# Performance work log

Hardware: AMD Instinct MI355X
Metric: run time of the kernel (lower is better)

## Reference

```python
import jax, jax.numpy as jnp
import numpy as np

B, N, D = 4, 1024, 1024
H = 16
RS, RC = 32, 32
MLP = int(D * 4.0)
EPS = 1e-6


def _ln(x):
    # LayerNorm with no scale/bias (flax defaults: eps=1e-6)
    m = jnp.mean(x, axis=-1, keepdims=True)
    v = jnp.mean(jnp.square(x - m), axis=-1, keepdims=True)
    return (x - m) * jax.lax.rsqrt(v + EPS)


def _rms(x, scale):
    rms = jnp.sqrt(jnp.mean(jnp.square(x), axis=-1, keepdims=True) + EPS)
    return scale * x / rms


def _modulate(x, shift, scale):
    return x * (1 + scale[:, None]) + shift[:, None]


def setup_inputs() -> dict:
    key = jax.random.key(0)
    ks = jax.random.split(key, 20)
    s = 0.02
    return {
        'x': jax.random.normal(ks[0], (B, N, D), jnp.float32),
        'c': jax.random.normal(ks[1], (B, D), jnp.float32),
        'cls_token': jax.random.normal(ks[2], (B, D), jnp.float32),
        'Wc': jax.random.normal(ks[3], (D, 6 * D), jnp.float32) * s,
        'bc': jax.random.normal(ks[4], (6 * D,), jnp.float32) * s,
        'Wqkv': jax.random.normal(ks[5], (D, 3 * D), jnp.float32) * s,
        'bqkv': jnp.zeros((3 * D,), jnp.float32),
        'Wo': jax.random.normal(ks[6], (D, D), jnp.float32) * s,
        'bo': jnp.zeros((D,), jnp.float32),
        'A_s': jax.random.normal(ks[7], (D, RS), jnp.float32) * s,
        'B_s': jax.random.normal(ks[8], (RS, D), jnp.float32) * s,
        'rms_s_scale': jnp.ones((D,), jnp.float32),
        'C_r': jax.random.normal(ks[9], (D, RC), jnp.float32) * s,
        'D_r': jax.random.normal(ks[10], (RC, D), jnp.float32) * s,
        'rms_c_scale': jnp.ones((D,), jnp.float32),
        'W1': jax.random.normal(ks[11], (D, MLP), jnp.float32) * s,
        'b1': jnp.zeros((MLP,), jnp.float32),
        'W2': jax.random.normal(ks[12], (MLP, D), jnp.float32) * s,
        'b2': jnp.zeros((D,), jnp.float32),
    }


def reference(x, c, cls_token, Wc, bc, Wqkv, bqkv, Wo, bo, A_s, B_s,
              rms_s_scale, C_r, D_r, rms_c_scale, W1, b1, W2, b2):
    hd = D // H
    # AdaLN conditioning
    c_proj = jax.nn.silu(c) @ Wc + bc                    # (B, 6D)
    shift_a, scale_a, gate_a, shift_m, scale_m, gate_m = jnp.split(c_proj, 6, axis=-1)

    # Self-attention branch
    x_norm = _modulate(_ln(x), shift_a, scale_a)         # (B, N, D)
    qkv = x_norm @ Wqkv + bqkv                           # (B, N, 3D)
    q, k, v = jnp.split(qkv, 3, axis=-1)
    q = q.reshape(B, N, H, hd).transpose(0, 2, 1, 3)     # (B, H, N, hd)
    k = k.reshape(B, N, H, hd).transpose(0, 2, 1, 3)
    v = v.reshape(B, N, H, hd).transpose(0, 2, 1, 3)
    attn_w = jax.nn.softmax(jnp.einsum('bhqd,bhkd->bhqk', q, k) * hd ** (-0.5), axis=-1)
    attn_out = jnp.einsum('bhqk,bhkd->bhqd', attn_w, v)
    attn_out = attn_out.transpose(0, 2, 1, 3).reshape(B, N, D)
    attn_out = attn_out @ Wo + bo
    Y = x + gate_a[:, None] * attn_out

    # Self-gram low-rank branch (residual)
    gram_s = (x @ A_s) @ B_s                             # (B, N, D)
    X_prime = _rms(gram_s, rms_s_scale) + Y

    # Cross-gram branch via CLS token (no residual)
    u_c = cls_token[:, :, None] * C_r[None]              # (B, D, RC)
    v_c = jnp.einsum('bnd,bdr->bnr', X_prime, u_c)       # (B, N, RC)
    gram_c = v_c @ D_r                                   # (B, N, D)
    Z = _rms(gram_c, rms_c_scale)

    # MLP branch
    z_norm = _modulate(_ln(Z), shift_m, scale_m)
    h = jax.nn.gelu(z_norm @ W1 + b1) @ W2 + b2
    return Z + gate_m[:, None] * h
```

## Files before the change

kernel.cpp:

```cpp
#include <hip/hip_runtime.h>
#include <stdint.h>

typedef float  f32x4  __attribute__((ext_vector_type(4)));
typedef int    i32x4  __attribute__((ext_vector_type(4)));
typedef __bf16 bf16x4 __attribute__((ext_vector_type(4)));

#define D_    1024
#define SIXD  6144
#define QSCALE 0.18033688011112042f

#define BAR() asm volatile("s_barrier" ::: "memory")

__device__ __forceinline__ void mfma16(const i32x4 &a, const i32x4 &b, f32x4 &c) {
  asm("v_mfma_f32_16x16x32_bf16 %0, %1, %2, %0" : "+v"(c) : "v"(a), "v"(b));
}

__device__ __forceinline__ void gload_lds16(const void* g, void* l) {
  __builtin_amdgcn_global_load_lds(
      (const __attribute__((address_space(1))) uint32_t*)g,
      (__attribute__((address_space(3))) uint32_t*)l, 16, 0, 0);
}

__global__ __launch_bounds__(256)
void cond_gemm(const float* __restrict__ c, const float* __restrict__ Wc,
               const float* __restrict__ bc, float* __restrict__ cproj)
{
  __shared__ float sc[4096];
  __shared__ float tp[8][4][32];
  int tid = threadIdx.x;
  for (int i = tid; i < 4096; i += 256) {
    float v = c[i];
    sc[i] = v / (1.f + __expf(-v));
  }
  __syncthreads();
  int colo = tid & 31, kseg = tid >> 5;
  int col = blockIdx.x * 32 + colo;
  float a0 = 0.f, a1 = 0.f, a2 = 0.f, a3 = 0.f;
  for (int k = kseg * 128; k < kseg * 128 + 128; k++) {
    float w = Wc[(size_t)k * SIXD + col];
    a0 += sc[k] * w; a1 += sc[1024 + k] * w;
    a2 += sc[2048 + k] * w; a3 += sc[3072 + k] * w;
  }
  tp[kseg][0][colo] = a0; tp[kseg][1][colo] = a1;
  tp[kseg][2][colo] = a2; tp[kseg][3][colo] = a3;
  __syncthreads();
  if (kseg == 0) {
#pragma unroll
    for (int b = 0; b < 4; b++) {
      float s = bc[col];
#pragma unroll
      for (int g = 0; g < 8; g++) s += tp[g][b][colo];
      cproj[b * SIXD + col] = s;
    }
  }
}

__global__ __launch_bounds__(256)
void transpose_all(const float* __restrict__ Wqkv, const float* __restrict__ Wo,
                   const float* __restrict__ W1, const float* __restrict__ W2,
                   __bf16* __restrict__ Wqkvt, __bf16* __restrict__ Wot,
                   __bf16* __restrict__ W1t, __bf16* __restrict__ W2t)
{
  __shared__ __bf16 t[64][65];
  int bid = blockIdx.x;
  const float* W; __bf16* Wt; int Kdim, Ndim, lb;
  if (bid < 768)       { W = Wqkv; Wt = Wqkvt; Kdim = 1024; Ndim = 3072; lb = bid; }
  else if (bid < 1024) { W = Wo;   Wt = Wot;   Kdim = 1024; Ndim = 1024; lb = bid - 768; }
  else if (bid < 2048) { W = W1;   Wt = W1t;   Kdim = 1024; Ndim = 4096; lb = bid - 1024; }
  else                 { W = W2;   Wt = W2t;   Kdim = 4096; Ndim = 1024; lb = bid - 2048; }
  int ntn = Ndim >> 6;
  int kt = lb / ntn, nt = lb % ntn;
  int tid = threadIdx.x;
  const float* src = W + (size_t)(kt * 64) * Ndim + nt * 64;
#pragma unroll
  for (int i = 0; i < 4; i++) {
    int k = i * 16 + (tid >> 4);
    int c4 = tid & 15;
    float4 v = ((const float4*)(src + (size_t)k * Ndim))[c4];
    t[k][c4 * 4 + 0] = (__bf16)v.x; t[k][c4 * 4 + 1] = (__bf16)v.y;
    t[k][c4 * 4 + 2] = (__bf16)v.z; t[k][c4 * 4 + 3] = (__bf16)v.w;
  }
  __syncthreads();
  __bf16* dst = Wt + (size_t)(nt * 64) * Kdim + kt * 64;
  int n = tid >> 2, ks = (tid & 3) * 16;
  bf16x4 o0, o1, o2, o3;
#pragma unroll
  for (int j = 0; j < 4; j++) {
    o0[j] = t[ks + j][n];      o1[j] = t[ks + 4 + j][n];
    o2[j] = t[ks + 8 + j][n];  o3[j] = t[ks + 12 + j][n];
  }
  __bf16* dp = dst + (size_t)n * Kdim + ks;
  *(bf16x4*)(dp) = o0; *(bf16x4*)(dp + 4) = o1;
  *(bf16x4*)(dp + 8) = o2; *(bf16x4*)(dp + 12) = o3;
}

__global__ __launch_bounds__(256)
void transpose_v(const __bf16* __restrict__ qkv, __bf16* __restrict__ Vt)
{
  __shared__ __bf16 t[32][33];
  int bid = blockIdx.x;
  int dt = bid & 1, nt = (bid >> 1) & 31, bh = bid >> 6;
  int b = bh >> 4, h = bh & 15;
  int x = threadIdx.x & 31, yq = threadIdx.x >> 5;
  const __bf16* src = qkv + ((size_t)(b * 1024 + nt * 32)) * 3072 + 2048 + h * 64 + dt * 32;
#pragma unroll
  for (int i = 0; i < 4; i++) {
    int row = yq * 4 + i;
    t[row][x] = src[(size_t)row * 3072 + x];
  }
  __syncthreads();
  __bf16* dst = Vt + ((size_t)(bh * 64 + dt * 32)) * 1024 + nt * 32;
#pragma unroll
  for (int i = 0; i < 4; i++) {
    int drow = yq * 4 + i;
    dst[(size_t)drow * 1024 + x] = t[x][drow];
  }
}

__global__ __launch_bounds__(256)
void ln_mod(const float* __restrict__ X, const float* __restrict__ cproj,
            int shift_off, int scale_off, __bf16* __restrict__ Out)
{
  int row = blockIdx.x;
  int b = row >> 10;
  int tid = threadIdx.x;
  const float4* xr = (const float4*)(X + (size_t)row * D_);
  float4 v = xr[tid];
  float s  = v.x + v.y + v.z + v.w;
  float s2 = v.x * v.x + v.y * v.y + v.z * v.z + v.w * v.w;
#pragma unroll
  for (int off = 1; off < 64; off <<= 1) {
    s  += __shfl_xor(s,  off, 64);
    s2 += __shfl_xor(s2, off, 64);
  }
  __shared__ float red[8];
  int wave = tid >> 6, lane = tid & 63;
  if (lane == 0) { red[wave] = s; red[4 + wave] = s2; }
  __syncthreads();
  s  = red[0] + red[1] + red[2] + red[3];
  s2 = red[4] + red[5] + red[6] + red[7];
  float mean = s * (1.f / D_);
  float var  = s2 * (1.f / D_) - mean * mean;
  float rstd = rsqrtf(var + 1e-6f);
  const float4* sh = (const float4*)(cproj + b * SIXD + shift_off);
  const float4* sc = (const float4*)(cproj + b * SIXD + scale_off);
  float4 shv = sh[tid], scv = sc[tid];
  bf16x4 o;
  o[0] = (__bf16)((v.x - mean) * rstd * (1.f + scv.x) + shv.x);
  o[1] = (__bf16)((v.y - mean) * rstd * (1.f + scv.y) + shv.y);
  o[2] = (__bf16)((v.z - mean) * rstd * (1.f + scv.z) + shv.z);
  o[3] = (__bf16)((v.w - mean) * rstd * (1.f + scv.w) + shv.w);
  *(bf16x4*)(Out + (size_t)row * D_ + tid * 4) = o;
}

template<int EPI, int NBUF>
__global__ __launch_bounds__(256)
void gemm_bt(const __bf16* __restrict__ A, const __bf16* __restrict__ Bt,
             const float* __restrict__ bias, const float* __restrict__ cproj,
             int gate_off, const float* __restrict__ resid,
             void* __restrict__ Cout, void* __restrict__ Cout2,
             void* __restrict__ Cout3, void* __restrict__ Cout4,
             int M, int N, int K, int SK)
{
  __shared__ __align__(16) __bf16 As[NBUF * 128 * 32];
  __shared__ __align__(16) __bf16 Bs[NBUF * 128 * 32];
  const int PD = NBUF - 1;
  int tilesN = N >> 7, tilesM = M >> 7;
  int npersk = tilesM * tilesN;
  int sk = blockIdx.x / npersk;
  int rest = blockIdx.x % npersk;
  int cpx = npersk >> 3;
  rest = (rest & 7) * cpx + (rest >> 3);
  int bm = rest / tilesN, bn = rest % tilesN;
  int Klen = K / SK, Kstart = sk * Klen;

  int tid = threadIdx.x;
  int lane = tid & 63, wave = tid >> 6;
  int lr = lane & 15, lg = lane >> 4;
  int wm = (wave >> 1) << 6, wn = (wave & 1) << 6;

  f32x4 acc[4][4] = {};

  int sr = tid >> 2, skb = tid & 3;
  int scol = ((skb ^ ((sr >> 1) & 3)) * 8);
  const __bf16* pa = A + (size_t)((bm << 7) + sr) * K + Kstart + scol;
  const __bf16* pb = Bt + (size_t)((bn << 7) + sr) * K + Kstart + scol;
  const size_t rstep = (size_t)64 * K;
  __bf16* la = As + tid * 8;
  __bf16* lb = Bs + tid * 8;

  auto STAGE = [&](int buf, int k0) {
    int bo = buf * 4096;
    gload_lds16(pa + k0, la + bo);
    gload_lds16(pa + rstep + k0, la + bo + 2048);
    gload_lds16(pb + k0, lb + bo);
    gload_lds16(pb + rstep + k0, lb + bo + 2048);
  };

  int nt = Klen >> 5;
#pragma unroll
  for (int p = 0; p < PD; p++) STAGE(p, p * 32);

  for (int t = 0; t < nt; t++) {
    if (t + PD < nt) STAGE((t + PD) % NBUF, (t + PD) * 32);
    int ahead = nt - 1 - t; if (ahead > PD) ahead = PD;
    if (ahead >= 3)      asm volatile("s_waitcnt vmcnt(12)" ::: "memory");
    else if (ahead == 2) asm volatile("s_waitcnt vmcnt(8)" ::: "memory");
    else if (ahead == 1) asm volatile("s_waitcnt vmcnt(4)" ::: "memory");
    else                 asm volatile("s_waitcnt vmcnt(0)" ::: "memory");
    BAR();
    const __bf16* Ac = As + (t % NBUF) * 4096;
    const __bf16* Bc = Bs + (t % NBUF) * 4096;
    i32x4 af[4], bfv[4];
#pragma unroll
    for (int m = 0; m < 4; m++) {
      int row = wm + m * 16 + lr;
      af[m] = *(const i32x4*)(Ac + row * 32 + ((lg ^ ((row >> 1) & 3)) * 8));
    }
#pragma unroll
    for (int n = 0; n < 4; n++) {
      int row = wn + n * 16 + lr;
      bfv[n] = *(const i32x4*)(Bc + row * 32 + ((lg ^ ((row >> 1) & 3)) * 8));
    }
    asm volatile("s_waitcnt lgkmcnt(0)" ::: "memory");
    __builtin_amdgcn_sched_barrier(0);
    BAR();
    __builtin_amdgcn_s_setprio(1);
#pragma unroll
    for (int m = 0; m < 4; m++)
#pragma unroll
      for (int n = 0; n < 4; n++)
        mfma16(af[m], bfv[n], acc[m][n]);
    __builtin_amdgcn_s_setprio(0);
  }
  asm volatile("s_waitcnt vmcnt(0)" ::: "memory");
  asm volatile("s_nop 7\n\ts_nop 7" ::);

  __bf16* Pp = nullptr;
  if (EPI == 3) {
    if (sk == 0)      Pp = (__bf16*)Cout;
    else if (sk == 1) Pp = (__bf16*)Cout2;
    else if (sk == 2) Pp = (__bf16*)Cout3;
    else              Pp = (__bf16*)Cout4;
  }

  int row0 = (bm << 7) + wm;
  int col0 = (bn << 7) + wn;
#pragma unroll
  for (int m = 0; m < 4; m++) {
#pragma unroll
    for (int n = 0; n < 4; n++) {
      int cc = col0 + n * 16 + lr;
      float bv = (EPI == 3) ? 0.f : bias[cc];
#pragma unroll
      for (int r = 0; r < 4; r++) {
        int row = row0 + m * 16 + (lg << 2) + r;
        float v = acc[m][n][r] + bv;
        size_t idx = (size_t)row * N + cc;
        if (EPI == 0) {
          ((__bf16*)Cout)[idx] = (__bf16)v;
        } else if (EPI == 1) {
          int b = row >> 10;
          float g = cproj[b * SIXD + gate_off + cc];
          ((float*)Cout)[idx] = resid[idx] + g * v;
        } else if (EPI == 2) {
          float u = 0.7978845608028654f * (v + 0.044715f * v * v * v);
          u = fminf(fmaxf(u, -15.f), 15.f);
          float e = __expf(2.f * u);
          float th = (e - 1.f) / (e + 1.f);
          ((__bf16*)Cout)[idx] = (__bf16)(0.5f * v * (1.f + th));
        } else if (EPI == 4) {
          float scq = (cc < 1024) ? QSCALE : 1.f;
          ((__bf16*)Cout)[idx] = (__bf16)(v * scq);
        } else {
          Pp[idx] = (__bf16)v;
        }
      }
    }
  }
}

template<int EPI>
__global__ __launch_bounds__(512, 2)
void gemm256(const __bf16* __restrict__ A, const __bf16* __restrict__ Bt,
             const float* __restrict__ bias,
             void* __restrict__ Cout, void* __restrict__ Cout2,
             void* __restrict__ Cout3, void* __restrict__ Cout4,
             int M, int N, int K, int SK)
{
  __shared__ __align__(16) __bf16 As[2 * 16384];
  __shared__ __align__(16) __bf16 Bs[2 * 16384];
  int tilesN = N >> 8, tilesM = M >> 8;
  int npersk = tilesM * tilesN;
  int sk = blockIdx.x / npersk;
  int rest = blockIdx.x % npersk;
  int cpx = npersk >> 3;
  rest = (rest & 7) * cpx + (rest >> 3);
  int bm = rest / tilesN, bn = rest % tilesN;
  int Klen = K / SK, Kstart = sk * Klen;
  int nt = Klen >> 6;

  int tid = threadIdx.x;
  int lane = tid & 63, wave = tid >> 6;
  int lr = lane & 15, lg = lane >> 4;
  int wr = wave >> 2, wc = wave & 3;

  f32x4 acc[8][4] = {};

  int srow = tid >> 3;
  int schunk = (tid & 7) ^ (srow & 7);
  const __bf16* pa = A  + (size_t)((bm << 8) + srow) * K + Kstart + schunk * 8;
  const __bf16* pb = Bt + (size_t)((bn << 8) + srow) * K + Kstart + schunk * 8;
  __bf16* la = As + tid * 8;
  __bf16* lb = Bs + tid * 8;

  auto SA = [&](int t, int h, int j) {
    gload_lds16(pa + (size_t)(h * 128 + j * 64) * K + t * 64,
                la + (t & 1) * 16384 + h * 8192 + j * 4096);
  };
  auto SB = [&](int t, int h, int j) {
    gload_lds16(pb + (size_t)(h * 128 + j * 64) * K + t * 64,
                lb + (t & 1) * 16384 + h * 8192 + j * 4096);
  };

  SA(0,0,0); SA(0,0,1); SA(0,1,0); SA(0,1,1);
  SB(0,0,0); SB(0,0,1); SB(0,1,0); SB(0,1,1);
  SB(1,0,0); SB(1,0,1); SB(1,1,0); SB(1,1,1);
  asm volatile("s_waitcnt vmcnt(4)" ::: "memory");
  BAR();

  int cc0 = ((lg ^ (lr & 7)) << 4);
  int cc1 = cc0 ^ 64;
  const char* aA = (const char*)As + (wr * 128 + lr) * 128;
  const char* aB = (const char*)Bs + (wc * 64 + lr) * 128;

  i32x4 af[4][2], b0[2][2], b1[2][2];
  for (int t = 0; t < nt; t++) {
    const char* Ab = aA + (t & 1) * 32768;
    const char* Bb = aB + (t & 1) * 32768;

#pragma unroll
    for (int m = 0; m < 4; m++) {
      af[m][0] = *(const i32x4*)(Ab + m * 2048 + cc0);
      af[m][1] = *(const i32x4*)(Ab + m * 2048 + cc1);
    }
#pragma unroll
    for (int n = 0; n < 2; n++) {
      b0[n][0] = *(const i32x4*)(Bb + n * 2048 + cc0);
      b0[n][1] = *(const i32x4*)(Bb + n * 2048 + cc1);
    }
    if (t + 1 < nt) { SA(t + 1, 0, 0); SA(t + 1, 0, 1); }
    BAR();
    asm volatile("s_waitcnt lgkmcnt(0)" ::: "memory");
    __builtin_amdgcn_sched_barrier(0);
    __builtin_amdgcn_s_setprio(1);
#pragma unroll
    for (int m = 0; m < 4; m++)
#pragma unroll
      for (int n = 0; n < 2; n++) {
        mfma16(af[m][0], b0[n][0], acc[m][n]);
        mfma16(af[m][1], b0[n][1], acc[m][n]);
      }
    __builtin_amdgcn_s_setprio(0);
    BAR();

#pragma unroll
    for (int n = 0; n < 2; n++) {
      b1[n][0] = *(const i32x4*)(Bb + 4096 + n * 2048 + cc0);
      b1[n][1] = *(const i32x4*)(Bb + 4096 + n * 2048 + cc1);
    }
    if (t + 1 < nt) { SA(t + 1, 1, 0); SA(t + 1, 1, 1); }
    BAR();
    asm volatile("s_waitcnt lgkmcnt(0)" ::: "memory");
    __builtin_amdgcn_sched_barrier(0);
    __builtin_amdgcn_s_setprio(1);
#pragma unroll
    for (int m = 0; m < 4; m++)
#pragma unroll
      for (int n = 0; n < 2; n++) {
        mfma16(af[m][0], b1[n][0], acc[m][2 + n]);
        mfma16(af[m][1], b1[n][1], acc[m][2 + n]);
      }
    __builtin_amdgcn_s_setprio(0);
    BAR();

#pragma unroll
    for (int m = 0; m < 4; m++) {
      af[m][0] = *(const i32x4*)(Ab + 8192 + m * 2048 + cc0);
      af[m][1] = *(const i32x4*)(Ab + 8192 + m * 2048 + cc1);
    }
    if (t + 2 < nt) { SB(t + 2, 0, 0); SB(t + 2, 0, 1); }
    BAR();
    asm volatile("s_waitcnt lgkmcnt(0)" ::: "memory");
    __builtin_amdgcn_sched_barrier(0);
    __builtin_amdgcn_s_setprio(1);
#pragma unroll
    for (int m = 0; m < 4; m++)
#pragma unroll
      for (int n = 0; n < 2; n++) {
        mfma16(af[m][0], b1[n][0], acc[4 + m][2 + n]);
        mfma16(af[m][1], b1[n][1], acc[4 + m][2 + n]);
      }
    __builtin_amdgcn_s_setprio(0);
    BAR();

    if (t + 2 < nt) {
      SB(t + 2, 1, 0); SB(t + 2, 1, 1);
      asm volatile("s_waitcnt vmcnt(4)" ::: "memory");
    } else {
      asm volatile("s_waitcnt vmcnt(0)" ::: "memory");
    }
    BAR();
    __builtin_amdgcn_s_setprio(1);
#pragma unroll
    for (int m = 0; m < 4; m++)
#pragma unroll
      for (int n = 0; n < 2; n++) {
        mfma16(af[m][0], b0[n][0], acc[4 + m][n]);
        mfma16(af[m][1], b0[n][1], acc[4 + m][n]);
      }
    __builtin_amdgcn_s_setprio(0);
    BAR();
  }
  asm volatile("s_nop 7\n\ts_nop 7" ::);

  __bf16* Pp = nullptr;
  if (EPI == 3) {
    if (sk == 0)      Pp = (__bf16*)Cout;
    else if (sk == 1) Pp = (__bf16*)Cout2;
    else if (sk == 2) Pp = (__bf16*)Cout3;
    else              Pp = (__bf16*)Cout4;
  }

  int row0 = (bm << 8) + wr * 128;
  int col0 = (bn << 8) + wc * 64;
#pragma unroll
  for (int m = 0; m < 8; m++) {
#pragma unroll
    for (int n = 0; n < 4; n++) {
      int cc = col0 + n * 16 + lr;
      float bv = (EPI == 3) ? 0.f : bias[cc];
#pragma unroll
      for (int r = 0; r < 4; r++) {
        int row = row0 + m * 16 + (lg << 2) + r;
        float v = acc[m][n][r] + bv;
        size_t idx = (size_t)row * N + cc;
        if (EPI == 2) {
          float u = 0.7978845608028654f * (v + 0.044715f * v * v * v);
          u = fminf(fmaxf(u, -15.f), 15.f);
          float e = __expf(2.f * u);
          float th = (e - 1.f) / (e + 1.f);
          ((__bf16*)Cout)[idx] = (__bf16)(0.5f * v * (1.f + th));
        } else if (EPI == 4) {
          float scq = (cc < 1024) ? QSCALE : 1.f;
          ((__bf16*)Cout)[idx] = (__bf16)(v * scq);
        } else {
          Pp[idx] = (__bf16)v;
        }
      }
    }
  }
}

__global__ __launch_bounds__(256)
void reduce_w2(const __bf16* __restrict__ P0, const __bf16* __restrict__ P1,
               const __bf16* __restrict__ P2, const __bf16* __restrict__ P3,
               const float* __restrict__ bias, const float* __restrict__ cproj,
               float* __restrict__ Out)
{
  int row = blockIdx.x;
  int b = row >> 10;
  int tid = threadIdx.x;
  size_t base = (size_t)row * D_ + tid * 4;
  bf16x4 a0 = *(const bf16x4*)(P0 + base);
  bf16x4 a1 = *(const bf16x4*)(P1 + base);
  bf16x4 a2 = *(const bf16x4*)(P2 + base);
  bf16x4 a3 = *(const bf16x4*)(P3 + base);
  f32x4 s;
#pragma unroll
  for (int i = 0; i < 4; i++)
    s[i] = ((float)a0[i] + (float)a1[i]) + ((float)a2[i] + (float)a3[i]);
  f32x4 bz = *(const f32x4*)(bias + tid * 4);
  f32x4 g  = *(const f32x4*)(cproj + b * SIXD + 5120 + tid * 4);
  f32x4 z  = *(const f32x4*)(Out + base);
  *(f32x4*)(Out + base) = z + g * (s + bz);
}

__global__ __launch_bounds__(512, 4)
void attn_flash(const __bf16* __restrict__ qkv, const __bf16* __restrict__ Vt,
                __bf16* __restrict__ O)
{
  __shared__ __align__(16) __bf16 Kl[2][64 * 64];
  __shared__ __align__(16) __bf16 Vl[2][64 * 64];
  __shared__ __align__(16) __bf16 Pl[8][16 * 64];

  int bid = ((blockIdx.x & 7) << 6) | (blockIdx.x >> 3);
  int qt = bid & 7, h = (bid >> 3) & 15, b = bid >> 7;
  int tid = threadIdx.x, wave = tid >> 6, lane = tid & 63;
  int lr = lane & 15, lg = lane >> 4;

  size_t tok0 = (size_t)b * 1024;
  int qrow = qt * 128 + wave * 16 + lr;
  const __bf16* qptr = qkv + (tok0 + qrow) * 3072 + h * 64;
  i32x4 qf0 = *(const i32x4*)(qptr + lg * 8);
  i32x4 qf1 = *(const i32x4*)(qptr + 32 + lg * 8);

  float l_acc[4] = {0.f, 0.f, 0.f, 0.f};
  f32x4 oacc[4] = {};

  const __bf16* kbase = qkv + tok0 * 3072 + 1024 + h * 64;
  const __bf16* vbase = Vt + ((size_t)(b * 16 + h) * 64) * 1024;

  int skey = tid >> 3, sdb = tid & 7;
  const __bf16* ksrc = kbase + (size_t)skey * 3072 + ((sdb ^ (skey & 7)) * 8);
  const __bf16* vsrc = vbase + (size_t)skey * 1024 + ((sdb ^ (skey & 7)) * 8);
  __bf16* klp = &Kl[0][0] + tid * 8;
  __bf16* vlp = &Vl[0][0] + tid * 8;
  __bf16* pl = &Pl[wave][0];

  auto STAGE = [&](int buf, int kk) {
    gload_lds16(ksrc + (size_t)kk * 3072, klp + buf * 4096);
    gload_lds16(vsrc + kk, vlp + buf * 4096);
  };

  STAGE(0, 0);
  int cur = 0;
  for (int k0 = 0; k0 < 1024; k0 += 64) {
    int kn = (k0 + 64 < 1024) ? (k0 + 64) : k0;
    STAGE(cur ^ 1, kn);
    asm volatile("s_waitcnt vmcnt(2)" ::: "memory");
    BAR();
    const __bf16* K_ = &Kl[cur][0];
    const __bf16* V_ = &Vl[cur][0];

    f32x4 s[4];
    __builtin_amdgcn_s_setprio(1);
#pragma unroll
    for (int n = 0; n < 4; n++) {
      int key = n * 16 + lr;
      int kx = key & 7;
      i32x4 kf0 = *(const i32x4*)(K_ + key * 64 + ((lg ^ kx) * 8));
      i32x4 kf1 = *(const i32x4*)(K_ + key * 64 + (((4 + lg) ^ kx) * 8));
      f32x4 sa = {0.f, 0.f, 0.f, 0.f};
      mfma16(qf0, kf0, sa);
      mfma16(qf1, kf1, sa);
      s[n] = sa;
    }
    __builtin_amdgcn_s_setprio(0);

#pragma unroll
    for (int n = 0; n < 4; n++)
#pragma unroll
      for (int r = 0; r < 4; r++)
        s[n][r] = exp2f(s[n][r]);
#pragma unroll
    for (int r = 0; r < 4; r++)
      l_acc[r] += (s[0][r] + s[1][r]) + (s[2][r] + s[3][r]);

#pragma unroll
    for (int n = 0; n < 4; n++)
#pragma unroll
      for (int r = 0; r < 4; r++) {
        int prow = lg * 4 + r;
        int key = n * 16 + lr;
        int idx = prow * 64 + (((key >> 3) ^ (prow & 7)) * 8) + (key & 7);
        pl[idx] = (__bf16)s[n][r];
      }
    asm volatile("s_waitcnt lgkmcnt(0)" ::: "memory");
    __builtin_amdgcn_sched_barrier(0);
    i32x4 pf0 = *(const i32x4*)(pl + lr * 64 + ((lg ^ (lr & 7)) * 8));
    i32x4 pf1 = *(const i32x4*)(pl + lr * 64 + (((4 + lg) ^ (lr & 7)) * 8));

    __builtin_amdgcn_s_setprio(1);
#pragma unroll
    for (int dt = 0; dt < 4; dt++) {
      int vrow = dt * 16 + lr, rx = vrow & 7;
      i32x4 vf0 = *(const i32x4*)(V_ + vrow * 64 + ((lg ^ rx) * 8));
      i32x4 vf1 = *(const i32x4*)(V_ + vrow * 64 + (((4 + lg) ^ rx) * 8));
      mfma16(pf0, vf0, oacc[dt]);
      mfma16(pf1, vf1, oacc[dt]);
    }
    __builtin_amdgcn_s_setprio(0);
    asm volatile("s_waitcnt lgkmcnt(0)" ::: "memory");
    __builtin_amdgcn_sched_barrier(0);
    BAR();
    cur ^= 1;
  }
  asm volatile("s_waitcnt vmcnt(0)" ::: "memory");
  asm volatile("s_nop 7\n\ts_nop 7" ::);

  float rinv[4];
#pragma unroll
  for (int r = 0; r < 4; r++) {
    float v = l_acc[r];
#pragma unroll
    for (int off = 1; off < 16; off <<= 1) v += __shfl_xor(v, off, 64);
    rinv[r] = 1.f / v;
  }

  int orow = qt * 128 + wave * 16 + (lg << 2);
#pragma unroll
  for (int dt = 0; dt < 4; dt++)
#pragma unroll
    for (int r = 0; r < 4; r++) {
      float v = oacc[dt][r] * rinv[r];
      O[(tok0 + orow + r) * 1024 + h * 64 + dt * 16 + lr] = (__bf16)v;
    }
}

__global__ __launch_bounds__(256)
void gram_fused(const float* __restrict__ X, const float* __restrict__ Y,
                const float* __restrict__ cls,
                const float* __restrict__ A_s, const float* __restrict__ B_s,
                const float* __restrict__ rms_s,
                const float* __restrict__ C_r, const float* __restrict__ D_r,
                const float* __restrict__ rms_c,
                const float* __restrict__ cproj,
                float* __restrict__ Z, __bf16* __restrict__ Znorm)
{
  __shared__ float xs[4][D_];
  __shared__ float tp[8][4][32];
  __shared__ float t1[4][32];
  __shared__ float red[4][4];
  __shared__ float red2[4][4][2];
  int row0 = blockIdx.x * 4;
  int b = row0 >> 10;
  int tid = threadIdx.x;
  int wv = tid >> 6;

  f32x4 cv = *(const f32x4*)(cls + (size_t)b * D_ + tid * 4);
  f32x4 yv[4];
#pragma unroll
  for (int rr = 0; rr < 4; rr++) {
    ((f32x4*)xs[rr])[tid] = *(const f32x4*)(X + (size_t)(row0 + rr) * D_ + tid * 4);
    yv[rr] = *(const f32x4*)(Y + (size_t)(row0 + rr) * D_ + tid * 4);
  }
  __syncthreads();

  {
    int r = tid & 31, seg = tid >> 5;
    float a0 = 0.f, a1 = 0.f, a2 = 0.f, a3 = 0.f;
    const float* ap = A_s + r;
    for (int d = seg * 128; d < seg * 128 + 128; d++) {
      float w = ap[d * 32];
      a0 += xs[0][d] * w; a1 += xs[1][d] * w;
      a2 += xs[2][d] * w; a3 += xs[3][d] * w;
    }
    tp[seg][0][r] = a0; tp[seg][1][r] = a1; tp[seg][2][r] = a2; tp[seg][3][r] = a3;
  }
  __syncthreads();
  if (tid < 128) {
    int rr = tid >> 5, r = tid & 31;
    float sv = 0.f;
#pragma unroll
    for (int g = 0; g < 8; g++) sv += tp[g][rr][r];
    t1[rr][r] = sv;
  }
  __syncthreads();

  f32x4 g[4] = {};
  for (int r = 0; r < 32; r++) {
    f32x4 bv = *(const f32x4*)(B_s + (size_t)r * D_ + tid * 4);
    g[0] += t1[0][r] * bv; g[1] += t1[1][r] * bv;
    g[2] += t1[2][r] * bv; g[3] += t1[3][r] * bv;
  }
  float ssl[4];
#pragma unroll
  for (int rr = 0; rr < 4; rr++)
    ssl[rr] = g[rr][0]*g[rr][0] + g[rr][1]*g[rr][1] + g[rr][2]*g[rr][2] + g[rr][3]*g[rr][3];
#pragma unroll
  for (int off = 1; off < 64; off <<= 1)
#pragma unroll
    for (int rr = 0; rr < 4; rr++) ssl[rr] += __shfl_xor(ssl[rr], off, 64);
  if ((tid & 63) == 0) {
#pragma unroll
    for (int rr = 0; rr < 4; rr++) red[wv][rr] = ssl[rr];
  }
  __syncthreads();
  {
    f32x4 scv = *(const f32x4*)(rms_s + tid * 4);
#pragma unroll
    for (int rr = 0; rr < 4; rr++) {
      float ss = red[0][rr] + red[1][rr] + red[2][rr] + red[3][rr];
      float rs = rsqrtf(ss * (1.f / D_) + 1e-6f);
      f32x4 xp = scv * g[rr] * rs + yv[rr];
      ((f32x4*)xs[rr])[tid] = xp * cv;
    }
  }
  __syncthreads();

  {
    int r = tid & 31, seg = tid >> 5;
    float a0 = 0.f, a1 = 0.f, a2 = 0.f, a3 = 0.f;
    const float* cp = C_r + r;
    for (int d = seg * 128; d < seg * 128 + 128; d++) {
      float w = cp[d * 32];
      a0 += xs[0][d] * w; a1 += xs[1][d] * w;
      a2 += xs[2][d] * w; a3 += xs[3][d] * w;
    }
    tp[seg][0][r] = a0; tp[seg][1][r] = a1; tp[seg][2][r] = a2; tp[seg][3][r] = a3;
  }
  __syncthreads();
  if (tid < 128) {
    int rr = tid >> 5, r = tid & 31;
    float sv = 0.f;
#pragma unroll
    for (int g2i = 0; g2i < 8; g2i++) sv += tp[g2i][rr][r];
    t1[rr][r] = sv;
  }
  __syncthreads();

  f32x4 g2[4] = {};
  for (int r = 0; r < 32; r++) {
    f32x4 bv = *(const f32x4*)(D_r + (size_t)r * D_ + tid * 4);
    g2[0] += t1[0][r] * bv; g2[1] += t1[1][r] * bv;
    g2[2] += t1[2][r] * bv; g2[3] += t1[3][r] * bv;
  }
#pragma unroll
  for (int rr = 0; rr < 4; rr++)
    ssl[rr] = g2[rr][0]*g2[rr][0] + g2[rr][1]*g2[rr][1] + g2[rr][2]*g2[rr][2] + g2[rr][3]*g2[rr][3];
#pragma unroll
  for (int off = 1; off < 64; off <<= 1)
#pragma unroll
    for (int rr = 0; rr < 4; rr++) ssl[rr] += __shfl_xor(ssl[rr], off, 64);
  if ((tid & 63) == 0) {
#pragma unroll
    for (int rr = 0; rr < 4; rr++) red[wv][rr] = ssl[rr];
  }
  __syncthreads();
  f32x4 z[4];
  {
    f32x4 scv = *(const f32x4*)(rms_c + tid * 4);
#pragma unroll
    for (int rr = 0; rr < 4; rr++) {
      float ss = red[0][rr] + red[1][rr] + red[2][rr] + red[3][rr];
      float rs = rsqrtf(ss * (1.f / D_) + 1e-6f);
      z[rr] = scv * g2[rr] * rs;
    }
  }

  float s1l[4], s2l[4];
#pragma unroll
  for (int rr = 0; rr < 4; rr++) {
    s1l[rr] = z[rr][0] + z[rr][1] + z[rr][2] + z[rr][3];
    s2l[rr] = z[rr][0]*z[rr][0] + z[rr][1]*z[rr][1] + z[rr][2]*z[rr][2] + z[rr][3]*z[rr][3];
  }
#pragma unroll
  for (int off = 1; off < 64; off <<= 1)
#pragma unroll
    for (int rr = 0; rr < 4; rr++) {
      s1l[rr] += __shfl_xor(s1l[rr], off, 64);
      s2l[rr] += __shfl_xor(s2l[rr], off, 64);
    }
  if ((tid & 63) == 0) {
#pragma unroll
    for (int rr = 0; rr < 4; rr++) { red2[wv][rr][0] = s1l[rr]; red2[wv][rr][1] = s2l[rr]; }
  }
  __syncthreads();
  f32x4 shv = *(const f32x4*)(cproj + b * SIXD + 3072 + tid * 4);
  f32x4 scm = *(const f32x4*)(cproj + b * SIXD + 4096 + tid * 4);
#pragma unroll
  for (int rr = 0; rr < 4; rr++) {
    float S  = red2[0][rr][0] + red2[1][rr][0] + red2[2][rr][0] + red2[3][rr][0];
    float S2 = red2[0][rr][1] + red2[1][rr][1] + red2[2][rr][1] + red2[3][rr][1];
    float mean = S * (1.f / D_);
    float var  = S2 * (1.f / D_) - mean * mean;
    float rstd = rsqrtf(var + 1e-6f);
    f32x4 zn = (z[rr] - mean) * rstd * (scm + 1.f) + shv;
    *(f32x4*)(Z + (size_t)(row0 + rr) * D_ + tid * 4) = z[rr];
    bf16x4 o;
#pragma unroll
    for (int i = 0; i < 4; i++) o[i] = (__bf16)zn[i];
    *(bf16x4*)(Znorm + (size_t)(row0 + rr) * D_ + tid * 4) = o;
  }
}

extern "C" void kernel_launch(void* const* d_in, const int* in_sizes, int n_in,
                              void* d_out, int out_size, void* d_ws, size_t ws_size,
                              hipStream_t stream)
{
  const float* x     = (const float*)d_in[0];
  const float* c     = (const float*)d_in[1];
  const float* cls   = (const float*)d_in[2];
  const float* Wc    = (const float*)d_in[3];
  const float* bc    = (const float*)d_in[4];
  const float* Wqkv  = (const float*)d_in[5];
  const float* bqkv  = (const float*)d_in[6];
  const float* Wo    = (const float*)d_in[7];
  const float* bo    = (const float*)d_in[8];
  const float* A_s   = (const float*)d_in[9];
  const float* B_s   = (const float*)d_in[10];
  const float* rms_s = (const float*)d_in[11];
  const float* C_r   = (const float*)d_in[12];
  const float* D_r   = (const float*)d_in[13];
  const float* rms_c = (const float*)d_in[14];
  const float* W1    = (const float*)d_in[15];
  const float* b1    = (const float*)d_in[16];
  const float* W2    = (const float*)d_in[17];
  const float* b2    = (const float*)d_in[18];
  float* out = (float*)d_out;

  float* ws = (float*)d_ws;
  __bf16* Wqkvt = (__bf16*)(ws + 0);
  __bf16* Wot   = (__bf16*)(ws + 1572864);
  __bf16* W1t   = (__bf16*)(ws + 2097152);
  __bf16* W2t   = (__bf16*)(ws + 4194304);
  float*  cproj = ws + 6291456;
  __bf16* xnorm = (__bf16*)(ws + 6316032);
  __bf16* qkv   = (__bf16*)(ws + 8413184);
  __bf16* Vt    = (__bf16*)(ws + 14704640);
  __bf16* h1    = (__bf16*)(ws + 8413184);
  __bf16* attno = (__bf16*)(ws + 16801792);
  float*  Ybuf  = ws + 18898944;
  __bf16* P0 = (__bf16*)(ws + 0);
  __bf16* P1 = (__bf16*)(ws + 2097152);
  __bf16* P2 = (__bf16*)(ws + 16801792);
  __bf16* P3 = (__bf16*)(ws + 18898944);

  cond_gemm<<<192, 256, 0, stream>>>(c, Wc, bc, cproj);
  transpose_all<<<3072, 256, 0, stream>>>(Wqkv, Wo, W1, W2, Wqkvt, Wot, W1t, W2t);
  ln_mod<<<4096, 256, 0, stream>>>(x, cproj, 0, 1024, xnorm);
  gemm256<4><<<192, 512, 0, stream>>>(xnorm, Wqkvt, bqkv,
                                      qkv, nullptr, nullptr, nullptr,
                                      4096, 3072, 1024, 1);
  transpose_v<<<4096, 256, 0, stream>>>(qkv, Vt);
  attn_flash<<<512, 512, 0, stream>>>(qkv, Vt, attno);
  gemm_bt<1, 4><<<256, 256, 0, stream>>>(attno, Wot, bo, cproj, 2048, x,
                                         Ybuf, nullptr, nullptr, nullptr,
                                         4096, 1024, 1024, 1);
  gram_fused<<<1024, 256, 0, stream>>>(x, Ybuf, cls, A_s, B_s, rms_s,
                                       C_r, D_r, rms_c, cproj, out, xnorm);
  gemm256<2><<<256, 512, 0, stream>>>(xnorm, W1t, b1,
                                      h1, nullptr, nullptr, nullptr,
                                      4096, 4096, 1024, 1);
  gemm256<3><<<256, 512, 0, stream>>>(h1, W2t, nullptr,
                                      P0, P1, P2, P3, 4096, 1024, 4096, 4);
  reduce_w2<<<4096, 256, 0, stream>>>(P0, P1, P2, P3, b2, cproj, out);
}
```

Before: 272.8 us.

## Restructure gemm256 main loop to prefetch LDS fragments and cut barriers

The gemm256 main loop is rewritten so A and B fragments for the next K-step are read from LDS at the end of the current step, and there are fewer barriers and no per-phase lgkmcnt waits. K length and K stride become template parameters, so the loop count and addresses are compile-time constants. Accumulators are moved to AGPRs through an MFMA variant with the 'a' constraint. The aim is to hide LDS latency and cut synchronisation stalls between MFMA phases. The cost is more register pressure and trickier vmcnt accounting for the double buffer.

```diff
diff --git a/kernel.cpp b/kernel.cpp
--- a/kernel.cpp
+++ b/kernel.cpp
@@ -13,6 +13,9 @@
 
 __device__ __forceinline__ void mfma16(const i32x4 &a, const i32x4 &b, f32x4 &c) {
   asm("v_mfma_f32_16x16x32_bf16 %0, %1, %2, %0" : "+v"(c) : "v"(a), "v"(b));
+}
+__device__ __forceinline__ void mfma16a(const i32x4 &a, const i32x4 &b, f32x4 &c) {
+  asm("v_mfma_f32_16x16x32_bf16 %0, %1, %2, %0" : "+a"(c) : "v"(a), "v"(b));
 }
 
 __device__ __forceinline__ void gload_lds16(const void* g, void* l) {
@@ -280,13 +283,13 @@
   }
 }
 
-template<int EPI>
+template<int EPI, int NT, int KD>
 __global__ __launch_bounds__(512, 2)
 void gemm256(const __bf16* __restrict__ A, const __bf16* __restrict__ Bt,
              const float* __restrict__ bias,
              void* __restrict__ Cout, void* __restrict__ Cout2,
              void* __restrict__ Cout3, void* __restrict__ Cout4,
-             int M, int N, int K, int SK)
+             int M, int N)
 {
   __shared__ __align__(16) __bf16 As[2 * 16384];
   __shared__ __align__(16) __bf16 Bs[2 * 16384];
@@ -297,8 +300,7 @@
   int cpx = npersk >> 3;
   rest = (rest & 7) * cpx + (rest >> 3);
   int bm = rest / tilesN, bn = rest % tilesN;
-  int Klen = K / SK, Kstart = sk * Klen;
-  int nt = Klen >> 6;
+  int Kstart = sk * (NT * 64);
 
   int tid = threadIdx.x;
   int lane = tid & 63, wave = tid >> 6;
@@ -309,23 +311,23 @@
 
   int srow = tid >> 3;
   int schunk = (tid & 7) ^ (srow & 7);
-  const __bf16* pa = A  + (size_t)((bm << 8) + srow) * K + Kstart + schunk * 8;
-  const __bf16* pb = Bt + (size_t)((bn << 8) + srow) * K + Kstart + schunk * 8;
+  const __bf16* pa = A  + (size_t)((bm << 8) + srow) * KD + Kstart + schunk * 8;
+  const __bf16* pb = Bt + (size_t)((bn << 8) + srow) * KD + Kstart + schunk * 8;
   __bf16* la = As + tid * 8;
   __bf16* lb = Bs + tid * 8;
 
-  auto SA = [&](int t, int h, int j) {
-    gload_lds16(pa + (size_t)(h * 128 + j * 64) * K + t * 64,
-                la + (t & 1) * 16384 + h * 8192 + j * 4096);
-  };
-  auto SB = [&](int t, int h, int j) {
-    gload_lds16(pb + (size_t)(h * 128 + j * 64) * K + t * 64,
-                lb + (t & 1) * 16384 + h * 8192 + j * 4096);
-  };
-
-  SA(0,0,0); SA(0,0,1); SA(0,1,0); SA(0,1,1);
-  SB(0,0,0); SB(0,0,1); SB(0,1,0); SB(0,1,1);
-  SB(1,0,0); SB(1,0,1); SB(1,1,0); SB(1,1,1);
+  gload_lds16(pa,                 la);
+  gload_lds16(pa + 64 * KD,       la + 4096);
+  gload_lds16(pa + 128 * KD,      la + 8192);
+  gload_lds16(pa + 192 * KD,      la + 12288);
+  gload_lds16(pb,                 lb);
+  gload_lds16(pb + 64 * KD,       lb + 4096);
+  gload_lds16(pb + 128 * KD,      lb + 8192);
+  gload_lds16(pb + 192 * KD,      lb + 12288);
+  gload_lds16(pb + 64,            lb + 16384);
+  gload_lds16(pb + 64 * KD + 64,  lb + 16384 + 4096);
+  gload_lds16(pb + 128 * KD + 64, lb + 16384 + 8192);
+  gload_lds16(pb + 192 * KD + 64, lb + 16384 + 12288);
   asm volatile("s_waitcnt vmcnt(4)" ::: "memory");
   BAR();
 
@@ -334,93 +336,112 @@
   const char* aA = (const char*)As + (wr * 128 + lr) * 128;
   const char* aB = (const char*)Bs + (wc * 64 + lr) * 128;
 
-  i32x4 af[4][2], b0[2][2], b1[2][2];
-  for (int t = 0; t < nt; t++) {
+  i32x4 alo[4][2], ahi[4][2], b0v[2][2], b1v[2][2];
+#pragma unroll
+  for (int m = 0; m < 4; m++) {
+    alo[m][0] = *(const i32x4*)(aA + m * 2048 + cc0);
+    alo[m][1] = *(const i32x4*)(aA + m * 2048 + cc1);
+  }
+#pragma unroll
+  for (int n = 0; n < 2; n++) {
+    b0v[n][0] = *(const i32x4*)(aB + n * 2048 + cc0);
+    b0v[n][1] = *(const i32x4*)(aB + n * 2048 + cc1);
+  }
+
+  for (int t = 0; t < NT; t++) {
     const char* Ab = aA + (t & 1) * 32768;
     const char* Bb = aB + (t & 1) * 32768;
-
-#pragma unroll
-    for (int m = 0; m < 4; m++) {
-      af[m][0] = *(const i32x4*)(Ab + m * 2048 + cc0);
-      af[m][1] = *(const i32x4*)(Ab + m * 2048 + cc1);
-    }
+    int nb = ((t + 1) & 1) * 16384;
+    int ob = (t & 1) * 16384;
+
 #pragma unroll
     for (int n = 0; n < 2; n++) {
-      b0[n][0] = *(const i32x4*)(Bb + n * 2048 + cc0);
-      b0[n][1] = *(const i32x4*)(Bb + n * 2048 + cc1);
-    }
-    if (t + 1 < nt) { SA(t + 1, 0, 0); SA(t + 1, 0, 1); }
-    BAR();
-    asm volatile("s_waitcnt lgkmcnt(0)" ::: "memory");
-    __builtin_amdgcn_sched_barrier(0);
+      b1v[n][0] = *(const i32x4*)(Bb + 4096 + n * 2048 + cc0);
+      b1v[n][1] = *(const i32x4*)(Bb + 4096 + n * 2048 + cc1);
+    }
+    if (t + 1 < NT) {
+      gload_lds16(pa + 64,            la + nb);
+      gload_lds16(pa + 128 * KD + 64, la + nb + 8192);
+    }
     __builtin_amdgcn_s_setprio(1);
 #pragma unroll
     for (int m = 0; m < 4; m++)
 #pragma unroll
       for (int n = 0; n < 2; n++) {
-        mfma16(af[m][0], b0[n][0], acc[m][n]);
-        mfma16(af[m][1], b0[n][1], acc[m][n]);
+        mfma16a(alo[m][0], b0v[n][0], acc[m][n]);
+        mfma16a(alo[m][1], b0v[n][1], acc[m][n]);
       }
     __builtin_amdgcn_s_setprio(0);
     BAR();
 
 #pragma unroll
-    for (int n = 0; n < 2; n++) {
-      b1[n][0] = *(const i32x4*)(Bb + 4096 + n * 2048 + cc0);
-      b1[n][1] = *(const i32x4*)(Bb + 4096 + n * 2048 + cc1);
-    }
-    if (t + 1 < nt) { SA(t + 1, 1, 0); SA(t + 1, 1, 1); }
-    BAR();
-    asm volatile("s_waitcnt lgkmcnt(0)" ::: "memory");
-    __builtin_amdgcn_sched_barrier(0);
+    for (int m = 0; m < 4; m++) {
+      ahi[m][0] = *(const i32x4*)(Ab + 8192 + m * 2048 + cc0);
+      ahi[m][1] = *(const i32x4*)(Ab + 8192 + m * 2048 + cc1);
+    }
+    if (t + 1 < NT) {
+      gload_lds16(pa + 64 * KD + 64,  la + nb + 4096);
+      gload_lds16(pa + 192 * KD + 64, la + nb + 12288);
+    }
     __builtin_amdgcn_s_setprio(1);
 #pragma unroll
     for (int m = 0; m < 4; m++)
 #pragma unroll
       for (int n = 0; n < 2; n++) {
-        mfma16(af[m][0], b1[n][0], acc[m][2 + n]);
-        mfma16(af[m][1], b1[n][1], acc[m][2 + n]);
+        mfma16a(alo[m][0], b1v[n][0], acc[m][2 + n]);
+        mfma16a(alo[m][1], b1v[n][1], acc[m][2 + n]);
       }
     __builtin_amdgcn_s_setprio(0);
     BAR();
 
-#pragma unroll
-    for (int m = 0; m < 4; m++) {
-      af[m][0] = *(const i32x4*)(Ab + 8192 + m * 2048 + cc0);
-      af[m][1] = *(const i32x4*)(Ab + 8192 + m * 2048 + cc1);
-    }
-    if (t + 2 < nt) { SB(t + 2, 0, 0); SB(t + 2, 0, 1); }
-    BAR();
-    asm volatile("s_waitcnt lgkmcnt(0)" ::: "memory");
-    __builtin_amdgcn_sched_barrier(0);
+    if (t + 2 < NT) {
+      gload_lds16(pb + 128,           lb + ob);
+      gload_lds16(pb + 64 * KD + 128, lb + ob + 4096);
+    }
     __builtin_amdgcn_s_setprio(1);
 #pragma unroll
     for (int m = 0; m < 4; m++)
 #pragma unroll
       for (int n = 0; n < 2; n++) {
-        mfma16(af[m][0], b1[n][0], acc[4 + m][2 + n]);
-        mfma16(af[m][1], b1[n][1], acc[4 + m][2 + n]);
+        mfma16a(ahi[m][0], b1v[n][0], acc[4 + m][2 + n]);
+        mfma16a(ahi[m][1], b1v[n][1], acc[4 + m][2 + n]);
       }
     __builtin_amdgcn_s_setprio(0);
+    if (t + 1 < NT) {
+      if (t + 2 < NT) asm volatile("s_waitcnt vmcnt(2)" ::: "memory");
+      else            asm volatile("s_waitcnt vmcnt(0)" ::: "memory");
+    }
     BAR();
 
-    if (t + 2 < nt) {
-      SB(t + 2, 1, 0); SB(t + 2, 1, 1);
-      asm volatile("s_waitcnt vmcnt(4)" ::: "memory");
-    } else {
-      asm volatile("s_waitcnt vmcnt(0)" ::: "memory");
-    }
-    BAR();
+    if (t + 2 < NT) {
+      gload_lds16(pb + 128 * KD + 128, lb + ob + 8192);
+      gload_lds16(pb + 192 * KD + 128, lb + ob + 12288);
+    }
     __builtin_amdgcn_s_setprio(1);
 #pragma unroll
     for (int m = 0; m < 4; m++)
 #pragma unroll
       for (int n = 0; n < 2; n++) {
-        mfma16(af[m][0], b0[n][0], acc[4 + m][n]);
-        mfma16(af[m][1], b0[n][1], acc[4 + m][n]);
+        mfma16a(ahi[m][0], b0v[n][0], acc[4 + m][n]);
+        mfma16a(ahi[m][1], b0v[n][1], acc[4 + m][n]);
       }
     __builtin_amdgcn_s_setprio(0);
+    if (t + 1 < NT) {
+      const char* An = aA + ((t + 1) & 1) * 32768;
+      const char* Bn = aB + ((t + 1) & 1) * 32768;
+#pragma unroll
+      for (int m = 0; m < 4; m++) {
+        alo[m][0] = *(const i32x4*)(An + m * 2048 + cc0);
+        alo[m][1] = *(const i32x4*)(An + m * 2048 + cc1);
+      }
+#pragma unroll
+      for (int n = 0; n < 2; n++) {
+        b0v[n][0] = *(const i32x4*)(Bn + n * 2048 + cc0);
+        b0v[n][1] = *(const i32x4*)(Bn + n * 2048 + cc1);
+      }
+    }
     BAR();
+    pa += 64; pb += 64;
   }
   asm volatile("s_nop 7\n\ts_nop 7" ::);
 
@@ -820,9 +841,9 @@
   cond_gemm<<<192, 256, 0, stream>>>(c, Wc, bc, cproj);
   transpose_all<<<3072, 256, 0, stream>>>(Wqkv, Wo, W1, W2, Wqkvt, Wot, W1t, W2t);
   ln_mod<<<4096, 256, 0, stream>>>(x, cproj, 0, 1024, xnorm);
-  gemm256<4><<<192, 512, 0, stream>>>(xnorm, Wqkvt, bqkv,
-                                      qkv, nullptr, nullptr, nullptr,
-                                      4096, 3072, 1024, 1);
+  gemm256<4, 16, 1024><<<192, 512, 0, stream>>>(xnorm, Wqkvt, bqkv,
+                                                qkv, nullptr, nullptr, nullptr,
+                                                4096, 3072);
   transpose_v<<<4096, 256, 0, stream>>>(qkv, Vt);
   attn_flash<<<512, 512, 0, stream>>>(qkv, Vt, attno);
   gemm_bt<1, 4><<<256, 256, 0, stream>>>(attno, Wot, bo, cproj, 2048, x,
@@ -830,10 +851,10 @@
                                          4096, 1024, 1024, 1);
   gram_fused<<<1024, 256, 0, stream>>>(x, Ybuf, cls, A_s, B_s, rms_s,
                                        C_r, D_r, rms_c, cproj, out, xnorm);
-  gemm256<2><<<256, 512, 0, stream>>>(xnorm, W1t, b1,
-                                      h1, nullptr, nullptr, nullptr,
-                                      4096, 4096, 1024, 1);
-  gemm256<3><<<256, 512, 0, stream>>>(h1, W2t, nullptr,
-                                      P0, P1, P2, P3, 4096, 1024, 4096, 4);
+  gemm256<2, 16, 1024><<<256, 512, 0, stream>>>(xnorm, W1t, b1,
+                                                h1, nullptr, nullptr, nullptr,
+                                                4096, 4096);
+  gemm256<3, 16, 4096><<<256, 512, 0, stream>>>(h1, W2t, nullptr,
+                                                P0, P1, P2, P3, 4096, 1024);
   reduce_w2<<<4096, 256, 0, stream>>>(P0, P1, P2, P3, b2, cproj, out);
 }
```

New measurement: 267.9 us. About the same (-1.8%).
